# Kernel tuning notes

Hardware: AMD Instinct MI355X
Metric: run time of the kernel (lower is better)

Reference implementation:

```python
import jax, jax.numpy as jnp
import numpy as np

INPUT_DIM = 6
HIDDEN = 256
NUM_CLASSES = 8
B = 16
V = 32768


def setup_inputs() -> dict:
    key = jax.random.key(0)
    ks = jax.random.split(key, 8)
    x = jax.random.normal(ks[0], (B, INPUT_DIM, V), dtype=jnp.float32)
    obj_idx = jax.random.randint(ks[1], (B,), 0, NUM_CLASSES)
    # Stacked per-class expert weights (Conv1d kernel_size=1 == pointwise linear)
    s1 = 1.0 / np.sqrt(INPUT_DIM)
    s2 = 1.0 / np.sqrt(HIDDEN)
    w1 = jax.random.uniform(ks[2], (NUM_CLASSES, HIDDEN, INPUT_DIM), jnp.float32, -s1, s1)
    b1 = jax.random.uniform(ks[3], (NUM_CLASSES, HIDDEN), jnp.float32, -s1, s1)
    w2 = jax.random.uniform(ks[4], (NUM_CLASSES, HIDDEN, HIDDEN), jnp.float32, -s2, s2)
    b2 = jax.random.uniform(ks[5], (NUM_CLASSES, HIDDEN), jnp.float32, -s2, s2)
    w3 = jax.random.uniform(ks[6], (NUM_CLASSES, 1, HIDDEN), jnp.float32, -s2, s2)
    b3 = jax.random.uniform(ks[7], (NUM_CLASSES, 1), jnp.float32, -s2, s2)
    return {"x": x, "obj_idx": obj_idx, "w1": w1, "b1": b1,
            "w2": w2, "b2": b2, "w3": w3, "b3": b3}


def reference(x, obj_idx, w1, b1, w2, b2, w3, b3):
    # Gather each sample's expert weights, then run the fused 3-layer pointwise
    # MLP over all B*V positions in one batched einsum per layer (no Python
    # loop over samples, unlike the original torch code).
    # x: [B, 6, V] -> out: [B, 1, V]
    h = jax.nn.relu(jnp.einsum('boi,biv->bov', w1[obj_idx], x) + b1[obj_idx][:, :, None])
    h = jax.nn.relu(jnp.einsum('boi,biv->bov', w2[obj_idx], h) + b2[obj_idx][:, :, None])
    out = jnp.einsum('boi,biv->bov', w3[obj_idx], h) + b3[obj_idx][:, :, None]
    return out
```

## Files before the change

### kernel.cpp

```cpp
#include <hip/hip_runtime.h>
#include <hip/hip_bf16.h>

typedef __bf16 bf16x8 __attribute__((ext_vector_type(8)));
typedef __bf16 bf16x4 __attribute__((ext_vector_type(4)));
typedef float  f32x4  __attribute__((ext_vector_type(4)));

#define V_TOTAL 32768
#define NT      512
#define NV      16
#define NBLK    512

#define NKLDS   2
#define W2_LDS  (NKLDS * 16384)
#define H1_LDS  32768
#define RED_LDS 2048
#define LDS_TOT (W2_LDS + H1_LDS + RED_LDS)

#define GLOAD_LDS16(g, l) __builtin_amdgcn_global_load_lds( \
    (const __attribute__((address_space(1))) void*)(g),     \
    (__attribute__((address_space(3))) void*)(l), 16, 0, 0)

__global__ void w2_to_bf16(const float* __restrict__ w2, __bf16* __restrict__ w2b) {
    int i = blockIdx.x * 256 + threadIdx.x;
    int e = i >> 16, q = i & 65535, c = q >> 3, j = q & 7;
    int kt = c >> 10, mt16 = (c >> 6) & 15, ko = (c >> 4) & 3, row = c & 15;
    w2b[i] = (__bf16)w2[e * 65536 + (mt16 * 16 + row) * 256 + kt * 32 + ko * 8 + j];
}

__global__ __launch_bounds__(NT) void fused_mlp(
    const float* __restrict__ x,  const int* __restrict__ obj,
    const float* __restrict__ w1, const float* __restrict__ b1,
    const float* __restrict__ b2, const float* __restrict__ w3,
    const float* __restrict__ b3, const __bf16* __restrict__ w2b,
    float* __restrict__ out)
{
    extern __shared__ __align__(16) char smem[];
    char*  w2s = smem;
    char*  h1t = smem + W2_LDS;
    float* red = (float*)(smem + W2_LDS + H1_LDS);

    const int t    = threadIdx.x;
    const int lane = t & 63;
    const int wv   = t >> 6;
    const int llo  = lane & 15;
    const int lhi  = lane >> 4;
    const int b    = blockIdx.x >> 5;
    const int g    = blockIdx.x & 31;
    const int e    = __builtin_amdgcn_readfirstlane(obj[b]);
    const __bf16* w2sw = w2b + (size_t)e * 65536;

    #pragma unroll
    for (int it = 0; it < 4; ++it) {
        int c0 = it * NT + wv * 64;
        GLOAD_LDS16(w2sw + c0 * 8 + lane * 8, w2s + c0 * 16);
    }

    bf16x8 aar[6][2];
    #pragma unroll
    for (int k2 = 0; k2 < 6; ++k2)
        #pragma unroll
        for (int mt = 0; mt < 2; ++mt) {
            int c = (2 + k2) * 1024 + (2 * wv + mt) * 64 + lane;
            aar[k2][mt] = *(const bf16x8*)(w2sw + c * 8);
        }

    const float* w1e = w1 + e * 1536;
    bf16x8 aa1[2];
    f32x4  b1f[2], bv[2], wf[2];
    #pragma unroll
    for (int mt2 = 0; mt2 < 2; ++mt2) {
        const int m0 = (2 * wv + mt2) * 16;
        bf16x8 v = {};
        if (lhi == 0)
            #pragma unroll
            for (int j = 0; j < 6; ++j) v[j] = (__bf16)w1e[(m0 + llo) * 6 + j];
        aa1[mt2] = v;
        b1f[mt2] = *(const f32x4*)(b1 + e * 256 + m0 + lhi * 4);
        bv[mt2]  = *(const f32x4*)(b2 + e * 256 + m0 + lhi * 4);
        wf[mt2]  = *(const f32x4*)(w3 + e * 256 + m0 + lhi * 4);
    }
    const float b3e = b3[e];
    const float* xe = x + (size_t)b * 6 * V_TOTAL;

    bf16x8 xf[4];
    auto load_x = [&](int ic) {
        #pragma unroll
        for (int pt = 0; pt < 4; ++pt) {
            bf16x8 v = {};
            #pragma unroll
            for (int i = 0; i < 6; ++i)
                v[i] = (__bf16)xe[i * V_TOTAL + (g * NV + ic) * 64 + pt * 16 + llo];
            xf[pt] = v;
        }
    };
    auto do_l1 = [&]() {
        #pragma unroll
        for (int mt2 = 0; mt2 < 2; ++mt2) {
            const int o = (2 * wv + mt2) * 2 + (lhi >> 1);
            char* wbase = h1t + (o >> 2) * 4096 + (o & 3) * 256
                              + llo * 16 + (lhi & 1) * 8;
            #pragma unroll
            for (int pt = 0; pt < 4; ++pt) {
                f32x4 h = __builtin_amdgcn_mfma_f32_16x16x32_bf16(
                    aa1[mt2], xf[pt], b1f[mt2], 0, 0, 0);
                bf16x4 pk;
                #pragma unroll
                for (int r = 0; r < 4; ++r) pk[r] = (__bf16)fmaxf(h[r], 0.f);
                *(bf16x4*)(wbase + pt * 1024) = pk;
            }
        }
    };

    load_x(0);

    for (int iv = 0; iv < NV; ++iv) {
        do_l1();
        if (iv + 1 < NV) load_x(iv + 1);
        __syncthreads();

        f32x4 acc[2][4];
        #pragma unroll
        for (int mt = 0; mt < 2; ++mt)
            #pragma unroll
            for (int nt = 0; nt < 4; ++nt) acc[mt][nt] = bv[mt];
        const char* abase = w2s + wv * 2048 + lane * 16;
        const char* bbase = h1t + lane * 16;
        #pragma unroll
        for (int kt = 0; kt < 2; ++kt) {
            bf16x8 bb[4];
            #pragma unroll
            for (int nt = 0; nt < 4; ++nt)
                bb[nt] = *(const bf16x8*)(bbase + kt * 4096 + nt * 1024);
            #pragma unroll
            for (int mt = 0; mt < 2; ++mt) {
                const bf16x8 aw = *(const bf16x8*)(abase + kt * 16384 + mt * 1024);
                #pragma unroll
                for (int nt = 0; nt < 4; ++nt)
                    acc[mt][nt] = __builtin_amdgcn_mfma_f32_16x16x32_bf16(
                        aw, bb[nt], acc[mt][nt], 0, 0, 0);
            }
        }
        #pragma unroll
        for (int k2 = 0; k2 < 6; ++k2) {
            bf16x8 bb[4];
            #pragma unroll
            for (int nt = 0; nt < 4; ++nt)
                bb[nt] = *(const bf16x8*)(bbase + (2 + k2) * 4096 + nt * 1024);
            #pragma unroll
            for (int mt = 0; mt < 2; ++mt)
                #pragma unroll
                for (int nt = 0; nt < 4; ++nt)
                    acc[mt][nt] = __builtin_amdgcn_mfma_f32_16x16x32_bf16(
                        aar[k2][mt], bb[nt], acc[mt][nt], 0, 0, 0);
        }

        float p[4];
        #pragma unroll
        for (int nt = 0; nt < 4; ++nt) {
            float s = 0.f;
            #pragma unroll
            for (int mt = 0; mt < 2; ++mt)
                #pragma unroll
                for (int j = 0; j < 4; ++j)
                    s = fmaf(wf[mt][j], fmaxf(acc[mt][nt][j], 0.f), s);
            s += __shfl_xor(s, 16, 64);
            s += __shfl_xor(s, 32, 64);
            p[nt] = s;
        }
        if (lane < 16)
            #pragma unroll
            for (int nt = 0; nt < 4; ++nt)
                red[wv * 64 + nt * 16 + lane] = p[nt];
        __syncthreads();

        if (t < 64) {
            float s = b3e;
            #pragma unroll
            for (int w8 = 0; w8 < 8; ++w8) s += red[w8 * 64 + t];
            out[(size_t)b * V_TOTAL + (g * NV + iv) * 64 + t] = s;
        }
    }
}

extern "C" void kernel_launch(void* const* d_in, const int* in_sizes, int n_in,
                              void* d_out, int out_size, void* d_ws, size_t ws_size,
                              hipStream_t stream) {
    const float* x   = (const float*)d_in[0];
    const int*   obj = (const int*)d_in[1];
    const float* w1  = (const float*)d_in[2];
    const float* b1  = (const float*)d_in[3];
    const float* w2  = (const float*)d_in[4];
    const float* b2  = (const float*)d_in[5];
    const float* w3  = (const float*)d_in[6];
    const float* b3  = (const float*)d_in[7];
    float*  out = (float*)d_out;
    __bf16* w2b = (__bf16*)d_ws;

    (void)hipFuncSetAttribute((const void*)fused_mlp,
                              hipFuncAttributeMaxDynamicSharedMemorySize, LDS_TOT);

    w2_to_bf16<<<2048, 256, 0, stream>>>(w2, w2b);
    fused_mlp<<<NBLK, NT, LDS_TOT, stream>>>(x, obj, w1, b1, b2, w3, b3, w2b, out);
}
```

Before: 86.50 us.

## Keep all W2 in registers, halve vertex tile to cut LDS footprint

Every wave now holds its full 256-wide K slice of W2 in registers instead of staging the first two K tiles in LDS. The vertex tile per iteration drops from 64 to 32, doubling the iteration count. LDS use falls from about 66KB to about 17KB, and the bias and w3 vectors are reloaded inside the loop instead of being kept live in registers. The goal is to remove LDS reads of W2 and allow more resident blocks per CU, at the cost of twice as many barriers and a lower MFMA-to-sync ratio per iteration.

```diff
diff --git a/kernel.cpp b/kernel.cpp
--- a/kernel.cpp
+++ b/kernel.cpp
@@ -7,18 +7,9 @@
 
 #define V_TOTAL 32768
 #define NT      512
-#define NV      16
+#define NV      32
 #define NBLK    512
 
-#define NKLDS   2
-#define W2_LDS  (NKLDS * 16384)
-#define H1_LDS  32768
-#define RED_LDS 2048
-#define LDS_TOT (W2_LDS + H1_LDS + RED_LDS)
-
-#define GLOAD_LDS16(g, l) __builtin_amdgcn_global_load_lds( \
-    (const __attribute__((address_space(1))) void*)(g),     \
-    (__attribute__((address_space(3))) void*)(l), 16, 0, 0)
 
 __global__ void w2_to_bf16(const float* __restrict__ w2, __bf16* __restrict__ w2b) {
     int i = blockIdx.x * 256 + threadIdx.x;
@@ -34,10 +25,8 @@
     const float* __restrict__ b3, const __bf16* __restrict__ w2b,
     float* __restrict__ out)
 {
-    extern __shared__ __align__(16) char smem[];
-    char*  w2s = smem;
-    char*  h1t = smem + W2_LDS;
-    float* red = (float*)(smem + W2_LDS + H1_LDS);
+    __shared__ __align__(16) char h1t[16384];
+    __shared__ float red[256];
 
     const int t    = threadIdx.x;
     const int lane = t & 63;
@@ -49,24 +38,20 @@
     const int e    = __builtin_amdgcn_readfirstlane(obj[b]);
     const __bf16* w2sw = w2b + (size_t)e * 65536;
 
+    bf16x8 aar[8][2];
     #pragma unroll
-    for (int it = 0; it < 4; ++it) {
-        int c0 = it * NT + wv * 64;
-        GLOAD_LDS16(w2sw + c0 * 8 + lane * 8, w2s + c0 * 16);
-    }
-
-    bf16x8 aar[6][2];
-    #pragma unroll
-    for (int k2 = 0; k2 < 6; ++k2)
+    for (int kt = 0; kt < 8; ++kt)
         #pragma unroll
         for (int mt = 0; mt < 2; ++mt) {
-            int c = (2 + k2) * 1024 + (2 * wv + mt) * 64 + lane;
-            aar[k2][mt] = *(const bf16x8*)(w2sw + c * 8);
+            int c = kt * 1024 + (2 * wv + mt) * 64 + lane;
+            aar[kt][mt] = *(const bf16x8*)(w2sw + c * 8);
         }
 
     const float* w1e = w1 + e * 1536;
+    const float* b1e = b1 + e * 256;
+    const float* b2e = b2 + e * 256;
+    const float* w3e = w3 + e * 256;
     bf16x8 aa1[2];
-    f32x4  b1f[2], bv[2], wf[2];
     #pragma unroll
     for (int mt2 = 0; mt2 < 2; ++mt2) {
         const int m0 = (2 * wv + mt2) * 16;
@@ -75,21 +60,18 @@
             #pragma unroll
             for (int j = 0; j < 6; ++j) v[j] = (__bf16)w1e[(m0 + llo) * 6 + j];
         aa1[mt2] = v;
-        b1f[mt2] = *(const f32x4*)(b1 + e * 256 + m0 + lhi * 4);
-        bv[mt2]  = *(const f32x4*)(b2 + e * 256 + m0 + lhi * 4);
-        wf[mt2]  = *(const f32x4*)(w3 + e * 256 + m0 + lhi * 4);
     }
     const float b3e = b3[e];
     const float* xe = x + (size_t)b * 6 * V_TOTAL;
 
-    bf16x8 xf[4];
+    bf16x8 xf[2];
     auto load_x = [&](int ic) {
         #pragma unroll
-        for (int pt = 0; pt < 4; ++pt) {
+        for (int pt = 0; pt < 2; ++pt) {
             bf16x8 v = {};
             #pragma unroll
             for (int i = 0; i < 6; ++i)
-                v[i] = (__bf16)xe[i * V_TOTAL + (g * NV + ic) * 64 + pt * 16 + llo];
+                v[i] = (__bf16)xe[i * V_TOTAL + (g * NV + ic) * 32 + pt * 16 + llo];
             xf[pt] = v;
         }
     };
@@ -97,12 +79,13 @@
         #pragma unroll
         for (int mt2 = 0; mt2 < 2; ++mt2) {
             const int o = (2 * wv + mt2) * 2 + (lhi >> 1);
-            char* wbase = h1t + (o >> 2) * 4096 + (o & 3) * 256
+            const f32x4 b1f = *(const f32x4*)(b1e + (2 * wv + mt2) * 16 + lhi * 4);
+            char* wbase = h1t + (o >> 2) * 2048 + (o & 3) * 256
                               + llo * 16 + (lhi & 1) * 8;
             #pragma unroll
-            for (int pt = 0; pt < 4; ++pt) {
+            for (int pt = 0; pt < 2; ++pt) {
                 f32x4 h = __builtin_amdgcn_mfma_f32_16x16x32_bf16(
-                    aa1[mt2], xf[pt], b1f[mt2], 0, 0, 0);
+                    aa1[mt2], xf[pt], b1f, 0, 0, 0);
                 bf16x4 pk;
                 #pragma unroll
                 for (int r = 0; r < 4; ++r) pk[r] = (__bf16)fmaxf(h[r], 0.f);
@@ -118,66 +101,52 @@
         if (iv + 1 < NV) load_x(iv + 1);
         __syncthreads();
 
-        f32x4 acc[2][4];
+        f32x4 acc[2][2];
         #pragma unroll
-        for (int mt = 0; mt < 2; ++mt)
-            #pragma unroll
-            for (int nt = 0; nt < 4; ++nt) acc[mt][nt] = bv[mt];
-        const char* abase = w2s + wv * 2048 + lane * 16;
+        for (int mt = 0; mt < 2; ++mt) {
+            const f32x4 bvv = *(const f32x4*)(b2e + (2 * wv + mt) * 16 + lhi * 4);
+            acc[mt][0] = bvv; acc[mt][1] = bvv;
+        }
         const char* bbase = h1t + lane * 16;
         #pragma unroll
-        for (int kt = 0; kt < 2; ++kt) {
-            bf16x8 bb[4];
-            #pragma unroll
-            for (int nt = 0; nt < 4; ++nt)
-                bb[nt] = *(const bf16x8*)(bbase + kt * 4096 + nt * 1024);
+        for (int kt = 0; kt < 8; ++kt) {
+            const bf16x8 bb0 = *(const bf16x8*)(bbase + kt * 2048);
+            const bf16x8 bb1 = *(const bf16x8*)(bbase + kt * 2048 + 1024);
             #pragma unroll
             for (int mt = 0; mt < 2; ++mt) {
-                const bf16x8 aw = *(const bf16x8*)(abase + kt * 16384 + mt * 1024);
-                #pragma unroll
-                for (int nt = 0; nt < 4; ++nt)
-                    acc[mt][nt] = __builtin_amdgcn_mfma_f32_16x16x32_bf16(
-                        aw, bb[nt], acc[mt][nt], 0, 0, 0);
+                acc[mt][0] = __builtin_amdgcn_mfma_f32_16x16x32_bf16(
+                    aar[kt][mt], bb0, acc[mt][0], 0, 0, 0);
+                acc[mt][1] = __builtin_amdgcn_mfma_f32_16x16x32_bf16(
+                    aar[kt][mt], bb1, acc[mt][1], 0, 0, 0);
             }
         }
+
+        float p[2];
         #pragma unroll
-        for (int k2 = 0; k2 < 6; ++k2) {
-            bf16x8 bb[4];
-            #pragma unroll
-            for (int nt = 0; nt < 4; ++nt)
-                bb[nt] = *(const bf16x8*)(bbase + (2 + k2) * 4096 + nt * 1024);
-            #pragma unroll
-            for (int mt = 0; mt < 2; ++mt)
-                #pragma unroll
-                for (int nt = 0; nt < 4; ++nt)
-                    acc[mt][nt] = __builtin_amdgcn_mfma_f32_16x16x32_bf16(
-                        aar[k2][mt], bb[nt], acc[mt][nt], 0, 0, 0);
-        }
-
-        float p[4];
-        #pragma unroll
-        for (int nt = 0; nt < 4; ++nt) {
+        for (int nt = 0; nt < 2; ++nt) {
             float s = 0.f;
             #pragma unroll
-            for (int mt = 0; mt < 2; ++mt)
+            for (int mt = 0; mt < 2; ++mt) {
+                const f32x4 wfv = *(const f32x4*)(w3e + (2 * wv + mt) * 16 + lhi * 4);
                 #pragma unroll
                 for (int j = 0; j < 4; ++j)
-                    s = fmaf(wf[mt][j], fmaxf(acc[mt][nt][j], 0.f), s);
+                    s = fmaf(wfv[j], fmaxf(acc[mt][nt][j], 0.f), s);
+            }
             s += __shfl_xor(s, 16, 64);
             s += __shfl_xor(s, 32, 64);
             p[nt] = s;
         }
         if (lane < 16)
             #pragma unroll
-            for (int nt = 0; nt < 4; ++nt)
-                red[wv * 64 + nt * 16 + lane] = p[nt];
+            for (int nt = 0; nt < 2; ++nt)
+                red[wv * 32 + nt * 16 + lane] = p[nt];
         __syncthreads();
 
-        if (t < 64) {
+        if (t < 32) {
             float s = b3e;
             #pragma unroll
-            for (int w8 = 0; w8 < 8; ++w8) s += red[w8 * 64 + t];
-            out[(size_t)b * V_TOTAL + (g * NV + iv) * 64 + t] = s;
+            for (int w8 = 0; w8 < 8; ++w8) s += red[w8 * 32 + t];
+            out[(size_t)b * V_TOTAL + (g * NV + iv) * 32 + t] = s;
         }
     }
 }
@@ -196,9 +165,6 @@
     float*  out = (float*)d_out;
     __bf16* w2b = (__bf16*)d_ws;
 
-    (void)hipFuncSetAttribute((const void*)fused_mlp,
-                              hipFuncAttributeMaxDynamicSharedMemorySize, LDS_TOT);
-
     w2_to_bf16<<<2048, 256, 0, stream>>>(w2, w2b);
-    fused_mlp<<<NBLK, NT, LDS_TOT, stream>>>(x, obj, w1, b1, b2, w3, b3, w2b, out);
+    fused_mlp<<<NBLK, NT, 0, stream>>>(x, obj, w1, b1, b2, w3, b3, w2b, out);
 }
```

Measured after the change: 93.84 us. +8.5%, slower.
